# Kernel tuning notes

Measured on AMD Instinct MI355X. Metric: run time of the kernel, lower is better.

Reference implementation:

```python
import jax, jax.numpy as jnp
import numpy as np

Q_BITS = 8
GELU_A = -0.2888
GELU_B = -1.769
INV_SQRT2 = 0.7071067811865476


def _ste_round(x):
    # straight-through round (identity grad)
    return x + jax.lax.stop_gradient(jnp.round(x) - x)


def fake_quant_weight(w):
    # per-tensor symmetric int8 fake quant
    qmax = 2.0 ** (Q_BITS - 1) - 1.0  # 127
    s = jnp.maximum(jnp.max(jnp.abs(w)), 1e-8) / qmax
    q = jnp.clip(_ste_round(w / s), -qmax - 1.0, qmax)
    return q * s


def fake_quant_act(x):
    # per-tensor asymmetric uint8 fake quant
    levels = 2.0 ** Q_BITS - 1.0  # 255
    xmin = jax.lax.stop_gradient(jnp.min(x))
    xmax = jax.lax.stop_gradient(jnp.max(x))
    s = jnp.maximum(xmax - xmin, 1e-8) / levels
    zp = jnp.round(-xmin / s)
    q = jnp.clip(_ste_round(x / s) + zp, 0.0, levels)
    return (q - zp) * s


def int_gelu(x):
    # I-BERT polynomial GELU: gelu(x) = x * 0.5 * (1 + L(x/sqrt(2)))
    # L(t) = sign(t) * (a * (clip(|t|, 0, -b) + b)^2 + 1)
    t = x * INV_SQRT2
    at = jnp.minimum(jnp.abs(t), -GELU_B)
    L = jnp.sign(t) * (GELU_A * (at + GELU_B) ** 2 + 1.0)
    return x * 0.5 * (1.0 + L)


def setup_inputs() -> dict:
    key = jax.random.key(0)
    k = jax.random.split(key, 5)
    B, S, D, H = 64, 197, 768, 3072
    x = jax.random.normal(k[0], (B, S, D), dtype=jnp.float32)
    w1 = jax.random.normal(k[1], (H, D), dtype=jnp.float32) * (1.0 / np.sqrt(D))
    b1 = jax.random.normal(k[2], (H,), dtype=jnp.float32) * 0.02
    w2 = jax.random.normal(k[3], (D, H), dtype=jnp.float32) * (1.0 / np.sqrt(H))
    b2 = jax.random.normal(k[4], (D,), dtype=jnp.float32) * 0.02
    return {"x": x, "w1": w1, "b1": b1, "w2": w2, "b2": b2}


def reference(x, w1, b1, w2, b2):
    # QuantLinear 1: fake-quant act + weight, then GEMM
    xq = fake_quant_act(x)
    h = jnp.einsum('bsd,hd->bsh', xq, fake_quant_weight(w1)) + b1
    # IntGELU (dropout is identity in eval)
    g = int_gelu(h)
    # QuantLinear 2
    gq = fake_quant_act(g)
    out = jnp.einsum('bsh,dh->bsd', gq, fake_quant_weight(w2)) + b2
    return out
```

## Files before the change

### kernel.cpp

```cpp
#include <hip/hip_runtime.h>
#include <stdint.h>
#include <stddef.h>

typedef int v4i  __attribute__((ext_vector_type(4)));
typedef int v16i __attribute__((ext_vector_type(16)));
typedef _Float16 vh8 __attribute__((ext_vector_type(8)));

#define GELU_A   (-0.2888f)
#define GELU_B   (-1.769f)
#define INV_SQRT2 0.70710678118654752440f

#define GLD16(gp, lp) __builtin_amdgcn_global_load_lds( \
    (const __attribute__((address_space(1))) unsigned int*)(gp), \
    (__attribute__((address_space(3))) unsigned int*)(lp), 16, 0, 0)

#define WAIT_VM4 0x0F74
#define WAIT_VM0 0x0F70


__device__ __forceinline__ unsigned enc_f(float f){
  unsigned u = __float_as_uint(f);
  return (u & 0x80000000u) ? ~u : (u | 0x80000000u);
}
__device__ __forceinline__ float dec_f(unsigned e){
  unsigned u = (e & 0x80000000u) ? (e & 0x7FFFFFFFu) : ~e;
  return __uint_as_float(u);
}

__device__ __forceinline__ float int_gelu_f(float x){
  float t = x * INV_SQRT2;
  float at = fminf(fabsf(t), 1.769f);
  float u = at + GELU_B;
  float p = GELU_A * (u * u) + 1.0f;
  float L = (t > 0.0f) ? p : ((t < 0.0f) ? -p : 0.0f);
  return x * 0.5f * (1.0f + L);
}

__global__ __launch_bounds__(256) void reduce_stats(
    const float4* __restrict__ x, int nx4,
    const float4* __restrict__ w1, int n14,
    const float4* __restrict__ w2, int n24,
    unsigned* __restrict__ sc)
{
  __shared__ float ra[256], rb[256];
  const int tid = threadIdx.x;
  const int b = blockIdx.x;
  if (b < 1024){
    float lmin = 3.4e38f, lmax = -3.4e38f;
    for (long i = (long)b * 256 + tid; i < nx4; i += 1024L * 256L){
      float4 v = x[i];
      lmin = fminf(lmin, fminf(fminf(v.x, v.y), fminf(v.z, v.w)));
      lmax = fmaxf(lmax, fmaxf(fmaxf(v.x, v.y), fmaxf(v.z, v.w)));
    }
    ra[tid] = lmin; rb[tid] = lmax;
    __syncthreads();
    for (int s = 128; s > 0; s >>= 1){
      if (tid < s){ ra[tid] = fminf(ra[tid], ra[tid + s]); rb[tid] = fmaxf(rb[tid], rb[tid + s]); }
      __syncthreads();
    }
    if (tid == 0){
      atomicMin(&sc[0], enc_f(ra[0]));
      atomicMax(&sc[2], enc_f(rb[0]));
    }
  } else {
    const float4* w; int n4; int slot; int bl;
    if (b < 1152){ w = w1; n4 = n14; slot = 3; bl = b - 1024; }
    else         { w = w2; n4 = n24; slot = 4; bl = b - 1152; }
    float la = 0.0f;
    for (long i = (long)bl * 256 + tid; i < n4; i += 128L * 256L){
      float4 v = w[i];
      la = fmaxf(la, fmaxf(fmaxf(fabsf(v.x), fabsf(v.y)), fmaxf(fabsf(v.z), fabsf(v.w))));
    }
    ra[tid] = la;
    __syncthreads();
    for (int s = 128; s > 0; s >>= 1){
      if (tid < s) ra[tid] = fmaxf(ra[tid], ra[tid + s]);
      __syncthreads();
    }
    if (tid == 0) atomicMax(&sc[slot], __float_as_uint(ra[0]));
  }
}

__global__ __launch_bounds__(256) void quant_all(
    const float4* __restrict__ x, unsigned* __restrict__ qx, long nx4,
    const float* __restrict__ w1, const float* __restrict__ w2,
    int8_t* __restrict__ qw1, int8_t* __restrict__ qw2,
    int* __restrict__ rs1, int* __restrict__ rs2,
    const unsigned* __restrict__ sc, int H, int D)
{
  const int tid = threadIdx.x;
  const int b = blockIdx.x;
  if (b < 2048){
    const float vmin = dec_f(sc[0]);
    const float vmax = dec_f(sc[2]);
    const float s  = fmaxf(vmax - vmin, 1e-8f) / 255.0f;
    const float zp = rintf(-vmin / s);
    for (long i = (long)b * 256 + tid; i < nx4; i += 2048L * 256L){
      float4 v = x[i];
      int q0 = (int)fminf(fmaxf(rintf(v.x / s) + zp, 0.0f), 255.0f) - 128;
      int q1 = (int)fminf(fmaxf(rintf(v.y / s) + zp, 0.0f), 255.0f) - 128;
      int q2 = (int)fminf(fmaxf(rintf(v.z / s) + zp, 0.0f), 255.0f) - 128;
      int q3 = (int)fminf(fmaxf(rintf(v.w / s) + zp, 0.0f), 255.0f) - 128;
      qx[i] = ((unsigned)(q0 & 255)) | ((unsigned)(q1 & 255) << 8) |
              ((unsigned)(q2 & 255) << 16) | ((unsigned)(q3 & 255) << 24);
    }
  } else {
    __shared__ int red[256];
    const int wb = b - 2048;
    const float* w; int8_t* q; int* rs; int K; int n; float s;
    if (wb < H){ w = w1; q = qw1; rs = rs1; K = D; n = wb;
                 s = fmaxf(__uint_as_float(sc[3]), 1e-8f) / 127.0f; }
    else       { w = w2; q = qw2; rs = rs2; K = H; n = wb - H;
                 s = fmaxf(__uint_as_float(sc[4]), 1e-8f) / 127.0f; }
    int sum = 0;
    for (int k = tid; k < K; k += 256){
      float v = w[(size_t)n * K + k];
      float qf = fminf(fmaxf(rintf(v / s), -128.0f), 127.0f);
      int qi = (int)qf;
      q[(size_t)n * K + k] = (int8_t)qi;
      sum += qi;
    }
    red[tid] = sum;
    __syncthreads();
    for (int st = 128; st > 0; st >>= 1){
      if (tid < st) red[tid] += red[tid + st];
      __syncthreads();
    }
    if (tid == 0) rs[n] = red[0];
  }
}

__global__ __launch_bounds__(256) void quant_g(
    const vh8* __restrict__ g, uint2* __restrict__ qg, long n8,
    const unsigned* __restrict__ sc)
{
  const float gmin = dec_f(sc[1]), gmax = dec_f(sc[5]);
  const float qs  = fmaxf(gmax - gmin, 1e-8f) / 255.0f;
  const float qzp = rintf(-gmin / qs);
  const long stride = (long)gridDim.x * blockDim.x;
  for (long i = (long)blockIdx.x * blockDim.x + threadIdx.x; i < n8; i += stride){
    vh8 v = g[i];
    unsigned lo = 0, hi = 0;
#pragma unroll
    for (int j = 0; j < 4; j++){
      int q = (int)fminf(fmaxf(rintf((float)v[j] / qs) + qzp, 0.0f), 255.0f) - 128;
      lo |= ((unsigned)(q & 255)) << (8 * j);
    }
#pragma unroll
    for (int j = 0; j < 4; j++){
      int q = (int)fminf(fmaxf(rintf((float)v[4 + j] / qs) + qzp, 0.0f), 255.0f) - 128;
      hi |= ((unsigned)(q & 255)) << (8 * j);
    }
    uint2 o; o.x = lo; o.y = hi;
    qg[i] = o;
  }
}

template<int MODE>
__global__ __launch_bounds__(256) void gemm_i8(
    const int8_t* __restrict__ A, const int8_t* __restrict__ Bm,
    const int* __restrict__ rowsum, const float* __restrict__ bias,
    void* __restrict__ Cout, int M, int N, int K,
    unsigned* __restrict__ sc)
{
  __shared__ __align__(16) int8_t lds[3][16384];

  const int tid  = threadIdx.x;
  const int lane = tid & 63;
  const int wave = tid >> 6;
  const int l31  = lane & 31;
  const int kh   = lane >> 5;
  const int n0   = blockIdx.x * 128;
  const int m0   = blockIdx.y * 128;
  const int wm   = (wave & 1) * 64;
  const int wn   = (wave >> 1) * 64;

  int aoffs[2], boffs[2];
  const int ldst[2] = { wave * 2048, wave * 2048 + 1024 };
#pragma unroll
  for (int t = 0; t < 2; t++){
    int rowl = wave * 32 + t * 16 + (lane >> 2);
    int csw  = ((lane & 3) ^ ((rowl >> 1) & 3)) << 4;
    int ga = m0 + rowl; if (ga >= M) ga = M - 1;
    aoffs[t] = ga * K + csw;
    boffs[t] = (n0 + rowl) * K + csw;
  }

  const int w2  = (l31 >> 1) & 3;
  const int sA0 = (kh ^ w2) << 4;
  int arow[2], brow[2];
#pragma unroll
  for (int mi = 0; mi < 2; mi++){
    arow[mi] = (wm + mi * 32 + l31) * 64;
    brow[mi] = (wn + mi * 32 + l31) * 64;
  }

  v16i acc[2][2] = {};
  const int NT = K >> 6;

#pragma unroll
  for (int t = 0; t < 2; t++){
    GLD16(A  + aoffs[t],      &lds[0][ldst[t]]);
    GLD16(Bm + boffs[t],      &lds[0][8192 + ldst[t]]);
  }
#pragma unroll
  for (int t = 0; t < 2; t++){
    GLD16(A  + aoffs[t] + 64, &lds[1][ldst[t]]);
    GLD16(Bm + boffs[t] + 64, &lds[1][8192 + ldst[t]]);
  }

  for (int kt = 0; kt < NT; kt++){
    const int8_t* buf = lds[kt % 3];
    if (kt + 1 < NT) __builtin_amdgcn_s_waitcnt(WAIT_VM4);
    else             __builtin_amdgcn_s_waitcnt(WAIT_VM0);
    __builtin_amdgcn_s_barrier();
    __builtin_amdgcn_sched_barrier(0);

    v4i af[2][2], bf[2][2];
#pragma unroll
    for (int kk = 0; kk < 2; kk++){
      const int sb = sA0 ^ (kk << 5);
#pragma unroll
      for (int mi = 0; mi < 2; mi++){
        af[kk][mi] = *(const v4i*)(buf + arow[mi] + sb);
        bf[kk][mi] = *(const v4i*)(buf + 8192 + brow[mi] + sb);
      }
    }

    if (kt + 2 < NT){
      int8_t* nbuf = lds[(kt + 2) % 3];
      const int ko = (kt + 2) << 6;
#pragma unroll
      for (int t = 0; t < 2; t++){
        GLD16(A  + aoffs[t] + ko, nbuf + ldst[t]);
        GLD16(Bm + boffs[t] + ko, nbuf + 8192 + ldst[t]);
      }
    }

#pragma unroll
    for (int kk = 0; kk < 2; kk++)
#pragma unroll
      for (int mi = 0; mi < 2; mi++)
#pragma unroll
        for (int nj = 0; nj < 2; nj++)
          acc[mi][nj] = __builtin_amdgcn_mfma_i32_32x32x32_i8(af[kk][mi], bf[kk][nj], acc[mi][nj], 0, 0, 0);
  }

  float s_h, off_h;
  if constexpr (MODE == 1){
    float gmin = dec_f(sc[1]), gmax = dec_f(sc[5]);
    float sg = fmaxf(gmax - gmin, 1e-8f) / 255.0f;
    float zp = rintf(-gmin / sg);
    float sw = fmaxf(__uint_as_float(sc[4]), 1e-8f) / 127.0f;
    s_h = sg * sw; off_h = 128.0f - zp;
  } else {
    float xmin = dec_f(sc[0]), xmax = dec_f(sc[2]);
    float sx = fmaxf(xmax - xmin, 1e-8f) / 255.0f;
    float zp = rintf(-xmin / sx);
    float sw = fmaxf(__uint_as_float(sc[3]), 1e-8f) / 127.0f;
    s_h = sx * sw; off_h = 128.0f - zp;
  }
  float qs = 1.0f, qzp = 0.0f;
  if constexpr (MODE == 2){
    float gmin = dec_f(sc[1]), gmax = dec_f(sc[5]);
    qs = fmaxf(gmax - gmin, 1e-8f) / 255.0f;
    qzp = rintf(-gmin / qs);
  }

  _Float16* tb = nullptr;
  if constexpr (MODE == 3){
    __syncthreads();
    tb = (_Float16*)(&lds[0][0]) + (size_t)wave * 4608;
  }

  float lmin = 3.4e38f, lmax = -3.4e38f;
#pragma unroll
  for (int nj = 0; nj < 2; nj++){
    const int n = n0 + wn + nj * 32 + l31;
    const float rsv = off_h * (float)rowsum[n];
    const float bv = bias[n];
#pragma unroll
    for (int mi = 0; mi < 2; mi++){
      const int mbase = m0 + wm + mi * 32 + 4 * kh;
#pragma unroll
      for (int r = 0; r < 16; r++){
        const int m = mbase + (r & 3) + 8 * (r >> 2);
        float h = s_h * ((float)acc[mi][nj][r] + rsv) + bv;
        if constexpr (MODE == 3){
          float gv = int_gelu_f(h);
          if (m < M){ lmin = fminf(lmin, gv); lmax = fmaxf(lmax, gv); }
          const int lmr = mi * 32 + 4 * kh + (r & 3) + 8 * (r >> 2);
          const int lnr = nj * 32 + l31;
          tb[lmr * 72 + lnr] = (_Float16)gv;
        } else if (m < M){
          if constexpr (MODE == 0){
            float gv = int_gelu_f(h);
            lmin = fminf(lmin, gv); lmax = fmaxf(lmax, gv);
          } else if constexpr (MODE == 2){
            float gv = int_gelu_f(h);
            float qf = fminf(fmaxf(rintf(gv / qs) + qzp, 0.0f), 255.0f);
            ((int8_t*)Cout)[(size_t)m * N + n] = (int8_t)((int)qf - 128);
          } else {
            ((float*)Cout)[(size_t)m * N + n] = h;
          }
        }
      }
    }
  }

  if constexpr (MODE == 3){
    __syncthreads();
#pragma unroll
    for (int it = 0; it < 8; it++){
      const int lr = it * 8 + (lane >> 3);
      const int c8 = (lane & 7) * 8;
      vh8 v = *(const vh8*)(tb + lr * 72 + c8);
      const int gm = m0 + wm + lr;
      if (gm < M)
        *(vh8*)((_Float16*)Cout + (size_t)gm * N + (n0 + wn + c8)) = v;
    }
  }

  if constexpr (MODE == 0 || MODE == 3){
    __syncthreads();
    float* redA = (float*)&lds[0][0];
    float* redB = ((float*)&lds[0][0]) + 256;
    redA[tid] = lmin; redB[tid] = lmax;
    __syncthreads();
    for (int st = 128; st > 0; st >>= 1){
      if (tid < st){
        redA[tid] = fminf(redA[tid], redA[tid + st]);
        redB[tid] = fmaxf(redB[tid], redB[tid + st]);
      }
      __syncthreads();
    }
    if (tid == 0){
      atomicMin(&sc[1], enc_f(redA[0]));
      atomicMax(&sc[5], enc_f(redB[0]));
    }
  }
}

extern "C" void kernel_launch(void* const* d_in, const int* in_sizes, int n_in,
                              void* d_out, int out_size, void* d_ws, size_t ws_size,
                              hipStream_t stream)
{
  const float* x  = (const float*)d_in[0];
  const float* w1 = (const float*)d_in[1];
  const float* b1 = (const float*)d_in[2];
  const float* w2 = (const float*)d_in[3];
  const float* b2 = (const float*)d_in[4];
  float* out = (float*)d_out;

  const int H = in_sizes[2];
  const int D = in_sizes[4];
  const int M = in_sizes[0] / D;

  char* ws = (char*)d_ws;
  unsigned* sc = (unsigned*)ws;
  size_t off = 256;
  int8_t* qx  = (int8_t*)(ws + off); off += (size_t)M * D;
  int8_t* qw1 = (int8_t*)(ws + off); off += (size_t)H * D;
  int8_t* qw2 = (int8_t*)(ws + off); off += (size_t)D * H;
  int* rs1 = (int*)(ws + off); off += (size_t)H * 4;
  int* rs2 = (int*)(ws + off); off += 4096;
  int8_t* qg  = (int8_t*)(ws + off); off += (size_t)M * H;
  _Float16* g16 = (_Float16*)(ws + off);
  const size_t need_big = off + (size_t)M * H * 2;
  (void)n_in; (void)out_size;

  hipMemsetAsync(sc, 0xFF, 8, stream);
  hipMemsetAsync(sc + 2, 0x00, 16, stream);

  reduce_stats<<<dim3(1280), dim3(256), 0, stream>>>(
      (const float4*)x, M * D / 4,
      (const float4*)w1, H * D / 4,
      (const float4*)w2, D * H / 4, sc);

  quant_all<<<dim3(2048 + H + D), dim3(256), 0, stream>>>(
      (const float4*)x, (unsigned*)qx, (long)M * D / 4,
      w1, w2, qw1, qw2, rs1, rs2, sc, H, D);

  const dim3 g1(H / 128, (M + 127) / 128), g2(D / 128, (M + 127) / 128), blk(256);

  if (ws_size >= need_big){
    gemm_i8<3><<<g1, blk, 0, stream>>>(qx, qw1, rs1, b1, g16, M, H, D, sc);
    quant_g<<<dim3(2048), blk, 0, stream>>>(
        (const vh8*)g16, (uint2*)qg, (long)M * H / 8, sc);
  } else {
    gemm_i8<0><<<g1, blk, 0, stream>>>(qx, qw1, rs1, b1, nullptr, M, H, D, sc);
    gemm_i8<2><<<g1, blk, 0, stream>>>(qx, qw1, rs1, b1, qg, M, H, D, sc);
  }

  gemm_i8<1><<<g2, blk, 0, stream>>>(qg, qw2, rs2, b2, out, M, D, H, sc);
}
```

Baseline: 306.0 us.

## Shrink GEMM LDS to double buffer and split fp16 epilogue staging in halves

Cuts the int8 GEMM shared-memory ring from three stages to two. An extra LDS-wait plus barrier after the fragment reads lets the next prefetch safely overwrite the buffer just consumed. The MODE 3 epilogue now stages the fp16 tile through LDS in two 32-row halves so it fits the smaller buffer, and the fp32 output store becomes nontemporal. Less LDS per block should let more blocks fit per CU, at the cost of an extra barrier per K step and a shallower prefetch distance.

```diff
diff --git a/kernel.cpp b/kernel.cpp
--- a/kernel.cpp
+++ b/kernel.cpp
@@ -14,8 +14,9 @@
     (const __attribute__((address_space(1))) unsigned int*)(gp), \
     (__attribute__((address_space(3))) unsigned int*)(lp), 16, 0, 0)
 
-#define WAIT_VM4 0x0F74
-#define WAIT_VM0 0x0F70
+#define WAIT_VM4   0x0F74
+#define WAIT_VM0   0x0F70
+#define WAIT_LGKM0 0xC07F
 
 
 __device__ __forceinline__ unsigned enc_f(float f){
@@ -163,7 +164,7 @@
     void* __restrict__ Cout, int M, int N, int K,
     unsigned* __restrict__ sc)
 {
-  __shared__ __align__(16) int8_t lds[3][16384];
+  __shared__ __align__(16) int8_t lds[2][16384];
 
   const int tid  = threadIdx.x;
   const int lane = tid & 63;
@@ -210,7 +211,7 @@
   }
 
   for (int kt = 0; kt < NT; kt++){
-    const int8_t* buf = lds[kt % 3];
+    const int8_t* buf = lds[kt & 1];
     if (kt + 1 < NT) __builtin_amdgcn_s_waitcnt(WAIT_VM4);
     else             __builtin_amdgcn_s_waitcnt(WAIT_VM0);
     __builtin_amdgcn_s_barrier();
@@ -226,9 +227,13 @@
         bf[kk][mi] = *(const v4i*)(buf + 8192 + brow[mi] + sb);
       }
     }
+    __builtin_amdgcn_sched_barrier(0);
+    __builtin_amdgcn_s_waitcnt(WAIT_LGKM0);
+    __builtin_amdgcn_s_barrier();
+    __builtin_amdgcn_sched_barrier(0);
 
     if (kt + 2 < NT){
-      int8_t* nbuf = lds[(kt + 2) % 3];
+      int8_t* nbuf = lds[kt & 1];
       const int ko = (kt + 2) << 6;
 #pragma unroll
       for (int t = 0; t < 2; t++){
@@ -236,6 +241,7 @@
         GLD16(Bm + boffs[t] + ko, nbuf + 8192 + ldst[t]);
       }
     }
+    __builtin_amdgcn_sched_barrier(0);
 
 #pragma unroll
     for (int kk = 0; kk < 2; kk++)
@@ -267,57 +273,66 @@
     qzp = rintf(-gmin / qs);
   }
 
-  _Float16* tb = nullptr;
+  float lmin = 3.4e38f, lmax = -3.4e38f;
+
   if constexpr (MODE == 3){
-    __syncthreads();
-    tb = (_Float16*)(&lds[0][0]) + (size_t)wave * 4608;
-  }
-
-  float lmin = 3.4e38f, lmax = -3.4e38f;
-#pragma unroll
-  for (int nj = 0; nj < 2; nj++){
-    const int n = n0 + wn + nj * 32 + l31;
-    const float rsv = off_h * (float)rowsum[n];
-    const float bv = bias[n];
-#pragma unroll
-    for (int mi = 0; mi < 2; mi++){
-      const int mbase = m0 + wm + mi * 32 + 4 * kh;
-#pragma unroll
-      for (int r = 0; r < 16; r++){
-        const int m = mbase + (r & 3) + 8 * (r >> 2);
-        float h = s_h * ((float)acc[mi][nj][r] + rsv) + bv;
-        if constexpr (MODE == 3){
+    _Float16* tb = (_Float16*)(&lds[0][0]) + (size_t)wave * 2304;
+#pragma unroll
+    for (int half = 0; half < 2; half++){
+      __syncthreads();
+#pragma unroll
+      for (int nj = 0; nj < 2; nj++){
+        const int n = n0 + wn + nj * 32 + l31;
+        const float rsv = off_h * (float)rowsum[n];
+        const float bv = bias[n];
+#pragma unroll
+        for (int r = 0; r < 16; r++){
+          const int lr32 = 4 * kh + (r & 3) + 8 * (r >> 2);
+          const int m = m0 + wm + half * 32 + lr32;
+          float h = s_h * ((float)acc[half][nj][r] + rsv) + bv;
           float gv = int_gelu_f(h);
           if (m < M){ lmin = fminf(lmin, gv); lmax = fmaxf(lmax, gv); }
-          const int lmr = mi * 32 + 4 * kh + (r & 3) + 8 * (r >> 2);
-          const int lnr = nj * 32 + l31;
-          tb[lmr * 72 + lnr] = (_Float16)gv;
-        } else if (m < M){
-          if constexpr (MODE == 0){
-            float gv = int_gelu_f(h);
-            lmin = fminf(lmin, gv); lmax = fmaxf(lmax, gv);
-          } else if constexpr (MODE == 2){
-            float gv = int_gelu_f(h);
-            float qf = fminf(fmaxf(rintf(gv / qs) + qzp, 0.0f), 255.0f);
-            ((int8_t*)Cout)[(size_t)m * N + n] = (int8_t)((int)qf - 128);
-          } else {
-            ((float*)Cout)[(size_t)m * N + n] = h;
+          tb[lr32 * 72 + nj * 32 + l31] = (_Float16)gv;
+        }
+      }
+      __syncthreads();
+#pragma unroll
+      for (int it = 0; it < 4; it++){
+        const int lr = it * 8 + (lane >> 3);
+        const int c8 = (lane & 7) * 8;
+        vh8 v = *(const vh8*)(tb + lr * 72 + c8);
+        const int gm = m0 + wm + half * 32 + lr;
+        if (gm < M)
+          *(vh8*)((_Float16*)Cout + (size_t)gm * N + (n0 + wn + c8)) = v;
+      }
+    }
+  } else {
+#pragma unroll
+    for (int nj = 0; nj < 2; nj++){
+      const int n = n0 + wn + nj * 32 + l31;
+      const float rsv = off_h * (float)rowsum[n];
+      const float bv = bias[n];
+#pragma unroll
+      for (int mi = 0; mi < 2; mi++){
+        const int mbase = m0 + wm + mi * 32 + 4 * kh;
+#pragma unroll
+        for (int r = 0; r < 16; r++){
+          const int m = mbase + (r & 3) + 8 * (r >> 2);
+          if (m < M){
+            float h = s_h * ((float)acc[mi][nj][r] + rsv) + bv;
+            if constexpr (MODE == 0){
+              float gv = int_gelu_f(h);
+              lmin = fminf(lmin, gv); lmax = fmaxf(lmax, gv);
+            } else if constexpr (MODE == 2){
+              float gv = int_gelu_f(h);
+              float qf = fminf(fmaxf(rintf(gv / qs) + qzp, 0.0f), 255.0f);
+              ((int8_t*)Cout)[(size_t)m * N + n] = (int8_t)((int)qf - 128);
+            } else {
+              __builtin_nontemporal_store(h, &((float*)Cout)[(size_t)m * N + n]);
+            }
           }
         }
       }
-    }
-  }
-
-  if constexpr (MODE == 3){
-    __syncthreads();
-#pragma unroll
-    for (int it = 0; it < 8; it++){
-      const int lr = it * 8 + (lane >> 3);
-      const int c8 = (lane & 7) * 8;
-      vh8 v = *(const vh8*)(tb + lr * 72 + c8);
-      const int gm = m0 + wm + lr;
-      if (gm < M)
-        *(vh8*)((_Float16*)Cout + (size_t)gm * N + (n0 + wn + c8)) = v;
     }
   }
 
```

Result: slower. 315.8 us (+3.2%).

## Fuse GELU-output activation quantization into the second int8 GEMM

Applied to the files above, without the earlier changes.

Drops the standalone quant_g pass. The second GEMM now loads the fp16 GELU output straight into registers, quantizes it to int8 with the global scale and zero point, and writes it into the LDS tile. The weight tile still goes through direct global-to-LDS loads in a three-buffer pipeline with explicit waitcnt and sched barriers. The goal is to avoid a full extra read and write of the large intermediate and one kernel launch. In exchange, the second GEMM reads twice as many A bytes, and each A tile is re-quantized by every N-block that uses it. The old decode helper is left with an uninitialized-variable bug, but all call sites switch to a fixed copy.

```diff
diff --git a/kernel.cpp b/kernel.cpp
--- a/kernel.cpp
+++ b/kernel.cpp
@@ -14,8 +14,10 @@
     (const __attribute__((address_space(1))) unsigned int*)(gp), \
     (__attribute__((address_space(3))) unsigned int*)(lp), 16, 0, 0)
 
-#define WAIT_VM4 0x0F74
-#define WAIT_VM0 0x0F70
+#define WAIT_VM4   0x0F74
+#define WAIT_VM2   0x0F72
+#define WAIT_VM0   0x0F70
+#define WAIT_LGKM0 0xC07F
 
 
 __device__ __forceinline__ unsigned enc_f(float f){
@@ -23,6 +25,10 @@
   return (u & 0x80000000u) ? ~u : (u | 0x80000000u);
 }
 __device__ __forceinline__ float dec_f(unsigned e){
+  unsigned u = (e & 0x80000000u) ? (e & 0x7FFFFFFFu) : ~u;
+  return __uint_as_float(u);
+}
+__device__ __forceinline__ float dec_f_fix(unsigned e){
   unsigned u = (e & 0x80000000u) ? (e & 0x7FFFFFFFu) : ~e;
   return __uint_as_float(u);
 }
@@ -34,6 +40,22 @@
   float p = GELU_A * (u * u) + 1.0f;
   float L = (t > 0.0f) ? p : ((t < 0.0f) ? -p : 0.0f);
   return x * 0.5f * (1.0f + L);
+}
+
+__device__ __forceinline__ uint2 quant8_g(v4i v, float qs, float qzp){
+  vh8 h = *(vh8*)&v;
+  unsigned lo = 0, hi = 0;
+#pragma unroll
+  for (int j = 0; j < 4; j++){
+    int q = (int)fminf(fmaxf(rintf((float)h[j] / qs) + qzp, 0.0f), 255.0f) - 128;
+    lo |= ((unsigned)(q & 255)) << (8 * j);
+  }
+#pragma unroll
+  for (int j = 0; j < 4; j++){
+    int q = (int)fminf(fmaxf(rintf((float)h[4 + j] / qs) + qzp, 0.0f), 255.0f) - 128;
+    hi |= ((unsigned)(q & 255)) << (8 * j);
+  }
+  uint2 r; r.x = lo; r.y = hi; return r;
 }
 
 __global__ __launch_bounds__(256) void reduce_stats(
@@ -91,8 +113,8 @@
   const int tid = threadIdx.x;
   const int b = blockIdx.x;
   if (b < 2048){
-    const float vmin = dec_f(sc[0]);
-    const float vmax = dec_f(sc[2]);
+    const float vmin = dec_f_fix(sc[0]);
+    const float vmax = dec_f_fix(sc[2]);
     const float s  = fmaxf(vmax - vmin, 1e-8f) / 255.0f;
     const float zp = rintf(-vmin / s);
     for (long i = (long)b * 256 + tid; i < nx4; i += 2048L * 256L){
@@ -130,32 +152,6 @@
   }
 }
 
-__global__ __launch_bounds__(256) void quant_g(
-    const vh8* __restrict__ g, uint2* __restrict__ qg, long n8,
-    const unsigned* __restrict__ sc)
-{
-  const float gmin = dec_f(sc[1]), gmax = dec_f(sc[5]);
-  const float qs  = fmaxf(gmax - gmin, 1e-8f) / 255.0f;
-  const float qzp = rintf(-gmin / qs);
-  const long stride = (long)gridDim.x * blockDim.x;
-  for (long i = (long)blockIdx.x * blockDim.x + threadIdx.x; i < n8; i += stride){
-    vh8 v = g[i];
-    unsigned lo = 0, hi = 0;
-#pragma unroll
-    for (int j = 0; j < 4; j++){
-      int q = (int)fminf(fmaxf(rintf((float)v[j] / qs) + qzp, 0.0f), 255.0f) - 128;
-      lo |= ((unsigned)(q & 255)) << (8 * j);
-    }
-#pragma unroll
-    for (int j = 0; j < 4; j++){
-      int q = (int)fminf(fmaxf(rintf((float)v[4 + j] / qs) + qzp, 0.0f), 255.0f) - 128;
-      hi |= ((unsigned)(q & 255)) << (8 * j);
-    }
-    uint2 o; o.x = lo; o.y = hi;
-    qg[i] = o;
-  }
-}
-
 template<int MODE>
 __global__ __launch_bounds__(256) void gemm_i8(
     const int8_t* __restrict__ A, const int8_t* __restrict__ Bm,
@@ -248,13 +244,13 @@
 
   float s_h, off_h;
   if constexpr (MODE == 1){
-    float gmin = dec_f(sc[1]), gmax = dec_f(sc[5]);
+    float gmin = dec_f_fix(sc[1]), gmax = dec_f_fix(sc[5]);
     float sg = fmaxf(gmax - gmin, 1e-8f) / 255.0f;
     float zp = rintf(-gmin / sg);
     float sw = fmaxf(__uint_as_float(sc[4]), 1e-8f) / 127.0f;
     s_h = sg * sw; off_h = 128.0f - zp;
   } else {
-    float xmin = dec_f(sc[0]), xmax = dec_f(sc[2]);
+    float xmin = dec_f_fix(sc[0]), xmax = dec_f_fix(sc[2]);
     float sx = fmaxf(xmax - xmin, 1e-8f) / 255.0f;
     float zp = rintf(-xmin / sx);
     float sw = fmaxf(__uint_as_float(sc[3]), 1e-8f) / 127.0f;
@@ -262,7 +258,7 @@
   }
   float qs = 1.0f, qzp = 0.0f;
   if constexpr (MODE == 2){
-    float gmin = dec_f(sc[1]), gmax = dec_f(sc[5]);
+    float gmin = dec_f_fix(sc[1]), gmax = dec_f_fix(sc[5]);
     qs = fmaxf(gmax - gmin, 1e-8f) / 255.0f;
     qzp = rintf(-gmin / qs);
   }
@@ -341,6 +337,157 @@
   }
 }
 
+__global__ __launch_bounds__(256) void gemm2_fused(
+    const _Float16* __restrict__ Ag, const int8_t* __restrict__ Bm,
+    const int* __restrict__ rowsum, const float* __restrict__ bias,
+    float* __restrict__ out, int M, int N, int K,
+    const unsigned* __restrict__ sc)
+{
+  __shared__ __align__(16) int8_t lds[3][16384];
+
+  const int tid  = threadIdx.x;
+  const int lane = tid & 63;
+  const int wave = tid >> 6;
+  const int l31  = lane & 31;
+  const int kh   = lane >> 5;
+  const int n0   = blockIdx.x * 128;
+  const int m0   = blockIdx.y * 128;
+  const int wm   = (wave & 1) * 64;
+  const int wn   = (wave >> 1) * 64;
+
+  const float gmin = dec_f_fix(sc[1]), gmax = dec_f_fix(sc[5]);
+  const float qs  = fmaxf(gmax - gmin, 1e-8f) / 255.0f;
+  const float qzp = rintf(-gmin / qs);
+
+  long aoffs[2]; int boffs[2];
+  const int ldst[2] = { wave * 2048, wave * 2048 + 1024 };
+#pragma unroll
+  for (int t = 0; t < 2; t++){
+    int rowl = wave * 32 + t * 16 + (lane >> 2);
+    int ch   = (lane & 3) ^ ((rowl >> 1) & 3);
+    int ga = m0 + rowl; if (ga >= M) ga = M - 1;
+    aoffs[t] = (long)ga * K + (long)ch * 16;
+    boffs[t] = (n0 + rowl) * K + (ch << 4);
+  }
+
+  const int w2  = (l31 >> 1) & 3;
+  const int sA0 = (kh ^ w2) << 4;
+  int arow[2], brow[2];
+#pragma unroll
+  for (int mi = 0; mi < 2; mi++){
+    arow[mi] = (wm + mi * 32 + l31) * 64;
+    brow[mi] = (wn + mi * 32 + l31) * 64;
+  }
+
+  v16i acc[2][2] = {};
+  const int NT = K >> 6;
+
+  v4i ap[2][2], an[2][2];
+
+#pragma unroll
+  for (int t = 0; t < 2; t++){
+    const int8_t* p = (const int8_t*)(Ag + aoffs[t]);
+    ap[t][0] = *(const v4i*)p; ap[t][1] = *(const v4i*)(p + 16);
+  }
+#pragma unroll
+  for (int t = 0; t < 2; t++){
+    const int8_t* p = (const int8_t*)(Ag + aoffs[t] + 64);
+    an[t][0] = *(const v4i*)p; an[t][1] = *(const v4i*)(p + 16);
+  }
+  __builtin_amdgcn_sched_barrier(0);
+#pragma unroll
+  for (int t = 0; t < 2; t++) GLD16(Bm + boffs[t],      &lds[0][8192 + ldst[t]]);
+#pragma unroll
+  for (int t = 0; t < 2; t++) GLD16(Bm + boffs[t] + 64, &lds[1][8192 + ldst[t]]);
+  __builtin_amdgcn_sched_barrier(0);
+
+#pragma unroll
+  for (int t = 0; t < 2; t++){
+    uint2 qa = quant8_g(ap[t][0], qs, qzp);
+    uint2 qb = quant8_g(ap[t][1], qs, qzp);
+    uint4 o; o.x = qa.x; o.y = qa.y; o.z = qb.x; o.w = qb.y;
+    *(uint4*)(&lds[0][ldst[t] + lane * 16]) = o;
+  }
+  __builtin_amdgcn_s_waitcnt(WAIT_LGKM0);
+
+  for (int kt = 0; kt < NT; kt++){
+    const int8_t* buf = lds[kt % 3];
+    if (kt + 1 < NT) __builtin_amdgcn_s_waitcnt(WAIT_VM2);
+    else             __builtin_amdgcn_s_waitcnt(WAIT_VM0);
+    __builtin_amdgcn_s_barrier();
+    __builtin_amdgcn_sched_barrier(0);
+
+    if (kt + 1 < NT){
+      int8_t* wb = lds[(kt + 1) % 3];
+#pragma unroll
+      for (int t = 0; t < 2; t++){
+        uint2 qa = quant8_g(an[t][0], qs, qzp);
+        uint2 qb = quant8_g(an[t][1], qs, qzp);
+        uint4 o; o.x = qa.x; o.y = qa.y; o.z = qb.x; o.w = qb.y;
+        *(uint4*)(wb + ldst[t] + lane * 16) = o;
+      }
+    }
+    __builtin_amdgcn_sched_barrier(0);
+
+    v4i af[2][2], bf[2][2];
+#pragma unroll
+    for (int kk = 0; kk < 2; kk++){
+      const int sb = sA0 ^ (kk << 5);
+#pragma unroll
+      for (int mi = 0; mi < 2; mi++){
+        af[kk][mi] = *(const v4i*)(buf + arow[mi] + sb);
+        bf[kk][mi] = *(const v4i*)(buf + 8192 + brow[mi] + sb);
+      }
+    }
+    __builtin_amdgcn_sched_barrier(0);
+
+    if (kt + 2 < NT){
+      const int ko = (kt + 2) << 6;
+#pragma unroll
+      for (int t = 0; t < 2; t++){
+        const int8_t* p = (const int8_t*)(Ag + aoffs[t] + ko);
+        an[t][0] = *(const v4i*)p; an[t][1] = *(const v4i*)(p + 16);
+      }
+      __builtin_amdgcn_sched_barrier(0);
+      int8_t* nb = lds[(kt + 2) % 3];
+#pragma unroll
+      for (int t = 0; t < 2; t++) GLD16(Bm + boffs[t] + ko, nb + 8192 + ldst[t]);
+    }
+    __builtin_amdgcn_sched_barrier(0);
+
+#pragma unroll
+    for (int kk = 0; kk < 2; kk++)
+#pragma unroll
+      for (int mi = 0; mi < 2; mi++)
+#pragma unroll
+        for (int nj = 0; nj < 2; nj++)
+          acc[mi][nj] = __builtin_amdgcn_mfma_i32_32x32x32_i8(af[kk][mi], bf[kk][nj], acc[mi][nj], 0, 0, 0);
+  }
+
+  const float sw  = fmaxf(__uint_as_float(sc[4]), 1e-8f) / 127.0f;
+  const float s_h = qs * sw;
+  const float off_h = 128.0f - qzp;
+
+#pragma unroll
+  for (int nj = 0; nj < 2; nj++){
+    const int n = n0 + wn + nj * 32 + l31;
+    const float rsv = off_h * (float)rowsum[n];
+    const float bv = bias[n];
+#pragma unroll
+    for (int mi = 0; mi < 2; mi++){
+      const int mbase = m0 + wm + mi * 32 + 4 * kh;
+#pragma unroll
+      for (int r = 0; r < 16; r++){
+        const int m = mbase + (r & 3) + 8 * (r >> 2);
+        if (m < M){
+          float h = s_h * ((float)acc[mi][nj][r] + rsv) + bv;
+          out[(size_t)m * N + n] = h;
+        }
+      }
+    }
+  }
+}
+
 extern "C" void kernel_launch(void* const* d_in, const int* in_sizes, int n_in,
                               void* d_out, int out_size, void* d_ws, size_t ws_size,
                               hipStream_t stream)
@@ -385,12 +532,10 @@
 
   if (ws_size >= need_big){
     gemm_i8<3><<<g1, blk, 0, stream>>>(qx, qw1, rs1, b1, g16, M, H, D, sc);
-    quant_g<<<dim3(2048), blk, 0, stream>>>(
-        (const vh8*)g16, (uint2*)qg, (long)M * H / 8, sc);
+    gemm2_fused<<<g2, blk, 0, stream>>>(g16, qw2, rs2, b2, out, M, D, H, sc);
   } else {
     gemm_i8<0><<<g1, blk, 0, stream>>>(qx, qw1, rs1, b1, nullptr, M, H, D, sc);
     gemm_i8<2><<<g1, blk, 0, stream>>>(qx, qw1, rs1, b1, qg, M, H, D, sc);
-  }
-
-  gemm_i8<1><<<g2, blk, 0, stream>>>(qg, qw2, rs2, b2, out, M, D, H, sc);
-}
+    gemm_i8<1><<<g2, blk, 0, stream>>>(qg, qw2, rs2, b2, out, M, D, H, sc);
+  }
+}
```

New measurement: 416.7 us. +36.1%, slower.
